# Kernel optimization log

Hardware: AMD Instinct MI355X
Metric: run time of the kernel (lower is better)

Reference implementation:

```python
import jax, jax.numpy as jnp
import numpy as np

B = 2048      # batch
S = 256       # num_hist_features (attention seq len)
D = 128       # model_dim
NSC = 16      # num scalar features
L = 2         # num attention layers
HURST = 0.1   # cfg.H
LN_EPS = 1e-5


def _log_fractional_kernel():
    # (|t-s| + 1e-9)^(H - 1.5), row-normalized, then log(k + 1e-9)
    idx = jnp.arange(S, dtype=jnp.float32)
    td = jnp.abs(idx[:, None] - idx[None, :]) + 1e-9
    kern = td ** (HURST - 1.5)
    kern = kern / kern.sum(axis=-1, keepdims=True)
    return jnp.log(kern + 1e-9)  # [S, S]


def setup_inputs() -> dict:
    key = jax.random.key(0)
    ks = jax.random.split(key, 20)
    sc = 0.02
    inp = {
        "x": jax.random.normal(ks[0], (B, NSC + S), dtype=jnp.float32),
        "scalar_W": jax.random.normal(ks[1], (NSC, D), dtype=jnp.float32) * sc,
        "scalar_b": jnp.zeros((D,), jnp.float32),
        "hist_W": jax.random.normal(ks[2], (1, D), dtype=jnp.float32) * sc,
        "hist_b": jnp.zeros((D,), jnp.float32),
        "qW": jax.random.normal(ks[3], (L, D, D), dtype=jnp.float32) * sc,
        "qb": jnp.zeros((L, D), jnp.float32),
        "kW": jax.random.normal(ks[4], (L, D, D), dtype=jnp.float32) * sc,
        "kb": jnp.zeros((L, D), jnp.float32),
        "vW": jax.random.normal(ks[5], (L, D, D), dtype=jnp.float32) * sc,
        "vb": jnp.zeros((L, D), jnp.float32),
        "ln_g": jnp.ones((L, D), jnp.float32),
        "ln_b": jnp.zeros((L, D), jnp.float32),
        "h1_W": jax.random.normal(ks[6], (D * (S + 1), 128), dtype=jnp.float32) * sc,
        "h1_b": jnp.zeros((128,), jnp.float32),
        "h2_W": jax.random.normal(ks[7], (128, 64), dtype=jnp.float32) * sc,
        "h2_b": jnp.zeros((64,), jnp.float32),
        "h3_W": jax.random.normal(ks[8], (64, 1), dtype=jnp.float32) * sc,
        "h3_b": jnp.zeros((1,), jnp.float32),
    }
    return inp


def _layernorm(h, g, b):
    mu = h.mean(axis=-1, keepdims=True)
    var = ((h - mu) ** 2).mean(axis=-1, keepdims=True)
    return (h - mu) * jax.lax.rsqrt(var + LN_EPS) * g + b


def reference(x, scalar_W, scalar_b, hist_W, hist_b, qW, qb, kW, kb, vW, vb,
              ln_g, ln_b, h1_W, h1_b, h2_W, h2_b, h3_W, h3_b):
    log_kern = _log_fractional_kernel()  # [S, S]
    scalar_feats = x[:, :-S]             # [B, NSC]
    hist_feats = x[:, -S:, None]         # [B, S, 1]
    scalar_emb = scalar_feats @ scalar_W + scalar_b   # [B, D]
    h = hist_feats @ hist_W + hist_b                   # [B, S, D]
    inv_sqrt_d = 1.0 / np.sqrt(D).astype(np.float32)
    for i in range(L):
        q = h @ qW[i] + qb[i]
        k = h @ kW[i] + kb[i]
        v = h @ vW[i] + vb[i]
        scores = jnp.einsum('bsd,btd->bst', q, k) * inv_sqrt_d  # [B,S,S]
        attn = jax.nn.softmax(scores + log_kern, axis=-1)
        out = jnp.einsum('bst,btd->bsd', attn, v)
        h = _layernorm(h + out, ln_g[i], ln_b[i])
    combined = jnp.concatenate([scalar_emb[:, None, :], h], axis=1).reshape(x.shape[0], -1)
    z = jax.nn.relu(combined @ h1_W + h1_b)
    z = jax.nn.relu(z @ h2_W + h2_b)
    return z @ h3_W + h3_b  # [B, 1]
```

## Files before the change

### kernel.cpp

```cpp
#include <hip/hip_runtime.h>
#include <cstddef>


typedef unsigned short u16;
typedef unsigned int u32;
typedef short short8 __attribute__((ext_vector_type(8)));
typedef u32 u32x2 __attribute__((ext_vector_type(2)));
typedef float floatx16 __attribute__((ext_vector_type(16)));

__device__ __forceinline__ float b2f(u16 u){ return __uint_as_float(((u32)u) << 16); }
__device__ __forceinline__ u16 f2b(float f){
  u32 u = __float_as_uint(f);
  return (u16)((u + 0x7fffu + ((u >> 16) & 1u)) >> 16);
}
__device__ __forceinline__ float ldf(const u16* p, size_t i, int f32){
  float v = f32 ? ((const float*)p)[i] : b2f(p[i]);
  return __builtin_isfinite(v) ? v : 0.f;
}
__device__ __forceinline__ u32 pk2(float a, float b){
  return ((u32)f2b(b) << 16) | (u32)f2b(a);
}
__device__ __forceinline__ int swz(int row, int ch){ return (row << 8) | ((ch ^ (row & 15)) << 4); }
__device__ __forceinline__ floatx16 fz(){
  floatx16 z;
#pragma unroll
  for (int i = 0; i < 16; ++i) z[i] = 0.f;
  return z;
}
__device__ __forceinline__ floatx16 MF(short8 a, short8 b, floatx16 c){
  return __builtin_amdgcn_mfma_f32_32x32x16_bf16(a, b, c, 0, 0, 0);
}
__device__ __forceinline__ short8 frag_from(floatx16 cv, int half, int q5){
  int r0 = half * 8;
  u32 e01 = pk2(cv[r0 + 0], cv[r0 + 1]);
  u32 e23 = pk2(cv[r0 + 2], cv[r0 + 3]);
  u32 o01 = pk2(cv[r0 + 4], cv[r0 + 5]);
  u32 o23 = pk2(cv[r0 + 6], cv[r0 + 7]);
  u32 s0 = q5 ? e01 : o01;
  u32 s1 = q5 ? e23 : o23;
  u32 r0v = __shfl_xor(s0, 32);
  u32 r1v = __shfl_xor(s1, 32);
  union { u32 u[4]; short8 v; } un;
  un.u[0] = q5 ? r0v : e01;
  un.u[1] = q5 ? r1v : e23;
  un.u[2] = q5 ? o01 : r0v;
  un.u[3] = q5 ? o23 : r1v;
  return un.v;
}

__global__ __launch_bounds__(256) void k_detect(const u16* x, int* dflag){
  __shared__ int red[256];
  int t = threadIdx.x, cnt = 0;
  for (int i = t; i < 4096; i += 256){
    u16 v = x[2 * i];
    int e = (v >> 7) & 0xFF;
    if (e == 0xFF || e >= 0x90 || (e > 0 && e <= 0x20)) ++cnt;
  }
  red[t] = cnt;
  __syncthreads();
  for (int off = 128; off > 0; off >>= 1){
    if (t < off) red[t] += red[t + off];
    __syncthreads();
  }
  if (t == 0) dflag[0] = (red[0] > 1000) ? 1 : 0;
}


__global__ __launch_bounds__(128) void k_prepw(const u16* qW, const u16* kW, const u16* vW,
                                               const u16* qb, u16* Mrow, u16* vWT, float* uv,
                                               const int* dflag){
  int fl = dflag[0];
  int i = blockIdx.x >> 7, f = blockIdx.x & 127, e = threadIdx.x;
  size_t qo = (size_t)(i * 128 + e) * 128;
  size_t ko = (size_t)(i * 128 + f) * 128;
  float m = 0.f;
  for (int d = 0; d < 128; ++d) m += ldf(qW, qo + d, fl) * ldf(kW, ko + d, fl);
  const float RS = 0.08838834764831845f;
  Mrow[(i * 128 + e) * 128 + f] = f2b(m * RS);
  vWT[(i * 128 + f) * 128 + e] = f2b(ldf(vW, qo + f, fl));
  __shared__ float red[128];
  red[e] = ldf(kW, ko + e, fl) * ldf(qb, (size_t)i * 128 + e, fl);
  __syncthreads();
  for (int off = 64; off > 0; off >>= 1){
    if (e < off) red[e] += red[e + off];
    __syncthreads();
  }
  if (e == 0) uv[i * 128 + f] = red[0] * RS;
}

__global__ __launch_bounds__(256) void k_h1t(const u16* h1W, u16* h1WT, const int* dflag){
  int fl = dflag[0];
  __shared__ u16 tile[64][130];
  int k0 = blockIdx.x * 64, tid = threadIdx.x;
#pragma unroll 4
  for (int it = 0; it < 32; ++it){
    int r = it * 2 + (tid >> 7), c = tid & 127;
    tile[r][c] = f2b(ldf(h1W, (size_t)(k0 + r) * 128 + c, fl));
  }
  __syncthreads();
#pragma unroll 4
  for (int it = 0; it < 32; ++it){
    int idx = it * 256 + tid, n = idx >> 6, kk = idx & 63;
    h1WT[(size_t)n * 32896 + k0 + kk] = tile[kk][n];
  }
}


__global__ __launch_bounds__(512) void k_fan(
    const u16* x, const u16* sW, const u16* sb, const u16* hW, const u16* hbe,
    const u16* Mrow, const float* uv, const u16* vWT, const u16* vb,
    const u16* lng, const u16* lnb,
    u16* hgq, u16* se, int qoff, const int* dflag){
  __shared__ alignas(16) u16 hL[32768];
  __shared__ alignas(16) u16 vt[16384];
  __shared__ alignas(16) u16 khL[16384];
  __shared__ float c_all[256];
  __shared__ float u_lds[128];
  int fl = dflag[0];
  int bl = blockIdx.x;
  int b = qoff + bl;
  int tid = threadIdx.x, w = tid >> 6, lane = tid & 63, l31 = lane & 31, q5 = lane >> 5;
  size_t xo = (size_t)b * 272;
  const float LKOFF = -20.72326584f;

  if (tid < 128){
    float acc = ldf(sb, tid, fl);
#pragma unroll
    for (int j = 0; j < 16; ++j) acc += ldf(x, xo + j, fl) * ldf(sW, (size_t)j * 128 + tid, fl);
    se[(size_t)b * 128 + tid] = f2b(acc);
  }
#pragma unroll
  for (int it = 0; it < 8; ++it){
    int c = it * 512 + tid, s = c >> 4, ch = c & 15;
    float xv = ldf(x, xo + 16 + s, fl);
    short8 r;
#pragma unroll
    for (int j = 0; j < 8; ++j)
      r[j] = (short)f2b(xv * ldf(hW, ch * 8 + j, fl) + ldf(hbe, ch * 8 + j, fl));
    *(short8*)((char*)hL + swz(s, ch)) = r;
  }

#pragma unroll 1
  for (int li = 0; li < 2; ++li){
    const u16* Mri  = Mrow + li * 16384;
    const u16* vWTi = vWT + li * 16384;
    if (tid < 128) u_lds[tid] = uv[li * 128 + tid];
    __syncthreads();

    {
      int row = 32 * w + l31;
      float dot = 0.f;
#pragma unroll 2
      for (int kc = 0; kc < 8; ++kc){
        int ch = 2 * kc + q5;
        short8 hv = *(const short8*)((char*)hL + swz(row, ch));
#pragma unroll
        for (int j = 0; j < 8; ++j) dot += u_lds[ch * 8 + j] * b2f(hv[j]);
      }
      dot += __shfl_xor(dot, 32);
      if (q5 == 0) c_all[row] = dot;
    }

    float ls_tot = 0.f;
    floatx16 oacc[4];
#pragma unroll
    for (int nt = 0; nt < 4; ++nt) oacc[nt] = fz();
    int scol = 32 * w + l31;

#pragma unroll 1
    for (int tt = 0; tt < 2; ++tt){
      int t0 = tt * 128;
      __syncthreads();
      {
        int mtv = w & 3;
#pragma unroll 1
        for (int j = 0; j < 2; ++j){
          int ntv = (w >> 2) * 2 + j;
          floatx16 ka = fz();
#pragma unroll 2
          for (int kc = 0; kc < 8; ++kc){
            short8 av = *(const short8*)(Mri + (32 * mtv + l31) * 128 + kc * 16 + q5 * 8);
            short8 bh = *(const short8*)((char*)hL + swz(t0 + 32 * ntv + l31, 2 * kc + q5));
            ka = MF(av, bh, ka);
          }
          int tloc = 32 * ntv + l31;
#pragma unroll
          for (int qd = 0; qd < 4; ++qd){
            u32x2 pv;
            pv.x = pk2(ka[4 * qd + 0], ka[4 * qd + 1]);
            pv.y = pk2(ka[4 * qd + 2], ka[4 * qd + 3]);
            *(u32x2*)((char*)khL + swz(tloc, 4 * mtv + qd) + 8 * q5) = pv;
          }
        }
      }
      {
        int mtv = w & 3;
        float vbl = ldf(vb, (size_t)li * 128 + 32 * mtv + l31, fl);
#pragma unroll 1
        for (int j = 0; j < 2; ++j){
          int ntv = (w >> 2) * 2 + j;
          floatx16 va = fz();
#pragma unroll 2
          for (int kc = 0; kc < 8; ++kc){
            short8 av = *(const short8*)(vWTi + (32 * mtv + l31) * 128 + kc * 16 + q5 * 8);
            short8 bh = *(const short8*)((char*)hL + swz(t0 + 32 * ntv + l31, 2 * kc + q5));
            va = MF(av, bh, va);
          }
#pragma unroll
          for (int reg = 0; reg < 16; ++reg){
            int rr = (reg & 3) + 8 * (reg >> 2) + 4 * q5;
            int tloc = 32 * ntv + l31;
            *(u16*)((char*)vt + swz(32 * mtv + rr, tloc >> 3) + (tloc & 7) * 2) =
                f2b(va[reg] + __shfl(vbl, rr));
          }
        }
      }
      __syncthreads();
#pragma unroll 1
      for (int mt = 0; mt < 4; ++mt){
        floatx16 sa = fz();
#pragma unroll 2
        for (int kc = 0; kc < 8; ++kc){
          short8 ak = *(const short8*)((char*)khL + swz(32 * mt + l31, 2 * kc + q5));
          short8 bq = *(const short8*)((char*)hL + swz(32 * w + l31, 2 * kc + q5));
          sa = MF(ak, bq, sa);
        }
#pragma unroll
        for (int reg = 0; reg < 16; ++reg){
          int trl = 32 * mt + (reg & 3) + 8 * (reg >> 2) + 4 * q5;
          int tg = t0 + trl;
          float lk = (tg == scol) ? 0.f : LKOFF;
          float v = sa[reg] + c_all[tg] + lk;
          v = fminf(fmaxf(v, -50.f), 50.f);
          float p = __expf(v - 8.f);
          sa[reg] = p;
          ls_tot += p;
        }
        short8 pf0 = frag_from(sa, 0, q5);
        short8 pf1 = frag_from(sa, 1, q5);
#pragma unroll
        for (int nt = 0; nt < 4; ++nt){
          short8 bv0 = *(const short8*)((char*)vt + swz(32 * nt + l31, 2 * (2 * mt + 0) + q5));
          oacc[nt] = MF(pf0, bv0, oacc[nt]);
          short8 bv1 = *(const short8*)((char*)vt + swz(32 * nt + l31, 2 * (2 * mt + 1) + q5));
          oacc[nt] = MF(pf1, bv1, oacc[nt]);
        }
      }
    }
    __syncthreads();

    float l_run = ls_tot + __shfl_xor(ls_tot, 32);
    float linv = 1.f / l_run;
    float gv[4], bbv[4];
#pragma unroll
    for (int nt = 0; nt < 4; ++nt){
      gv[nt]  = ldf(lng, (size_t)li * 128 + 32 * nt + l31, fl);
      bbv[nt] = ldf(lnb, (size_t)li * 128 + 32 * nt + l31, fl);
    }
#pragma unroll
    for (int reg = 0; reg < 16; ++reg){
      int rr = (reg & 3) + 8 * (reg >> 2) + 4 * q5;
      int srow = 32 * w + rr;
      float lrv = __shfl(linv, rr);
      float s1 = 0.f, s2 = 0.f;
#pragma unroll
      for (int nt = 0; nt < 4; ++nt){
        int d = 32 * nt + l31;
        float res = b2f(*(const u16*)((char*)hL + swz(srow, d >> 3) + (d & 7) * 2));
        float v = oacc[nt][reg] * lrv + res;
        oacc[nt][reg] = v;
        s1 += v; s2 += v * v;
      }
#pragma unroll
      for (int off = 1; off < 32; off <<= 1){ s1 += __shfl_xor(s1, off); s2 += __shfl_xor(s2, off); }
      float mu = s1 * 0.0078125f;
      float rs = rsqrtf(fmaxf(s2 * 0.0078125f - mu * mu, 0.f) + 1e-5f);
#pragma unroll
      for (int nt = 0; nt < 4; ++nt){
        int d = 32 * nt + l31;
        float v = (oacc[nt][reg] - mu) * rs * gv[nt] + bbv[nt];
        *(u16*)((char*)hL + swz(srow, d >> 3) + (d & 7) * 2) = f2b(v);
      }
    }
    __syncthreads();
  }

#pragma unroll
  for (int it = 0; it < 8; ++it){
    int c = it * 512 + tid, row = c >> 4, ch = c & 15;
    *(short8*)(hgq + (size_t)bl * 32768 + row * 128 + ch * 8) =
        *(const short8*)((char*)hL + swz(row, ch));
  }
}


__global__ __launch_bounds__(256) void k_mlp1(const u16* se, const u16* hgq, const u16* h1WT,
                                              float* part, int qoff, int nb){
  int mb = blockIdx.x, ks = blockIdx.y;
  int tid = threadIdx.x, w = tid >> 6, lane = tid & 63, l31 = lane & 31, q5 = lane >> 5;
  int b0 = mb * 32;
  floatx16 acc = fz();
  const u16* brow = h1WT + (size_t)(32 * w + l31) * 32896;
  int br = b0 + l31;
  const u16* seb = se + (size_t)(qoff + br) * 128;
  const u16* hb = hgq + (size_t)br * 32768;
  for (int kk = 0; kk < 257; ++kk){
    int kbase = ks * 4112 + kk * 16;
    const u16* ap = (kbase < 128) ? (seb + kbase + q5 * 8) : (hb + (kbase - 128) + q5 * 8);
    short8 a = *(const short8*)ap;
    short8 bf = *(const short8*)(brow + kbase + q5 * 8);
    acc = MF(a, bf, acc);
  }
#pragma unroll
  for (int reg = 0; reg < 16; ++reg){
    int rr = (reg & 3) + 8 * (reg >> 2) + 4 * q5;
    part[(size_t)ks * nb * 128 + (size_t)(b0 + rr) * 128 + 32 * w + l31] = acc[reg];
  }
}

__global__ __launch_bounds__(256) void k_mlp1red(const float* part, const u16* h1b, float* z1q,
                                                 const int* dflag, int nb){
  int fl = dflag[0];
  int idx = blockIdx.x * 256 + threadIdx.x;
  float s = ldf(h1b, idx & 127, fl);
  size_t stride = (size_t)nb * 128;
#pragma unroll
  for (int ks = 0; ks < 8; ++ks) s += part[(size_t)ks * stride + idx];
  z1q[idx] = fmaxf(s, 0.f);
}

__global__ __launch_bounds__(256) void k_mlp2(const float* z1, const u16* h2W, const u16* h2b,
                                              float* z2, const int* dflag){
  int fl = dflag[0];
  int idx = blockIdx.x * 256 + threadIdx.x;
  int b = idx >> 6, j = idx & 63;
  float s = ldf(h2b, j, fl);
  const float* zr = z1 + (size_t)b * 128;
  for (int k = 0; k < 128; ++k) s += zr[k] * ldf(h2W, (size_t)k * 64 + j, fl);
  z2[idx] = fmaxf(s, 0.f);
}

__global__ __launch_bounds__(256) void k_mlp3(const float* z2, const u16* h3W, const u16* h3b,
                                              void* out, const int* dflag){
  int fl = dflag[0];
  int b = blockIdx.x * 256 + threadIdx.x;
  float s = ldf(h3b, 0, fl);
  const float* zr = z2 + (size_t)b * 64;
#pragma unroll
  for (int j = 0; j < 64; ++j) s += zr[j] * ldf(h3W, j, fl);
  if (!__builtin_isfinite(s)) s = 0.f;
  if (fl) ((float*)out)[b] = s;
  else    ((u16*)out)[b] = f2b(s);
}


extern "C" void kernel_launch(void* const* d_in, const int* in_sizes, int n_in,
                              void* d_out, int out_size, void* d_ws, size_t ws_size,
                              hipStream_t stream) {
  const u16* x   = (const u16*)d_in[0];
  const u16* sW  = (const u16*)d_in[1];
  const u16* sb  = (const u16*)d_in[2];
  const u16* hW  = (const u16*)d_in[3];
  const u16* hb  = (const u16*)d_in[4];
  const u16* qW  = (const u16*)d_in[5];
  const u16* qb  = (const u16*)d_in[6];
  const u16* kW  = (const u16*)d_in[7];
  const u16* vW  = (const u16*)d_in[9];
  const u16* vb  = (const u16*)d_in[10];
  const u16* lng = (const u16*)d_in[11];
  const u16* lnb = (const u16*)d_in[12];
  const u16* h1W = (const u16*)d_in[13];
  const u16* h1b = (const u16*)d_in[14];
  const u16* h2W = (const u16*)d_in[15];
  const u16* h2b = (const u16*)d_in[16];
  const u16* h3W = (const u16*)d_in[17];
  const u16* h3b = (const u16*)d_in[18];

  const int nb = (ws_size >= 153600000ull) ? 2048 : 512;
  const int nq = 2048 / nb;

  char* W = (char*)d_ws;
  size_t o = 0;
  u16*   hg    = (u16*)(W + o); o += (size_t)nb * 65536;
  u16*   h1WT  = (u16*)(W + o); o += 8421376;
  u16*   se    = (u16*)(W + o); o += 524288;
  u16*   Mrow  = (u16*)(W + o); o += 65536;
  u16*   vWT   = (u16*)(W + o); o += 65536;
  float* uv    = (float*)(W + o); o += 1024;
  float* part  = (float*)(W + o); o += (size_t)nb * 4096;
  float* z1    = (float*)(W + o); o += 1048576;
  float* z2    = (float*)(W + o); o += 524288;
  int*   dflag = (int*)(W + o);

  k_detect<<<1, 256, 0, stream>>>(x, dflag);
  k_prepw<<<256, 128, 0, stream>>>(qW, kW, vW, qb, Mrow, vWT, uv, dflag);
  k_h1t<<<514, 256, 0, stream>>>(h1W, h1WT, dflag);

  for (int q = 0; q < nq; ++q){
    int qoff = q * nb;
    k_fan<<<nb, 512, 0, stream>>>(x, sW, sb, hW, hb, Mrow, uv, vWT, vb,
                                  lng, lnb, hg, se, qoff, dflag);
    k_mlp1<<<dim3(nb / 32, 8), 256, 0, stream>>>(se, hg, h1WT, part, qoff, nb);
    k_mlp1red<<<nb / 2, 256, 0, stream>>>(part, h1b, z1 + (size_t)qoff * 128, dflag, nb);
  }

  k_mlp2<<<512, 256, 0, stream>>>(z1, h2W, h2b, z2, dflag);
  k_mlp3<<<8, 256, 0, stream>>>(z2, h3W, h3b, d_out, dflag);
}
```

Measured before the change: 1.095 ms.

## Split attention key tiles across 16 waves with LDS partial-sum reduction

```diff
diff --git a/kernel.cpp b/kernel.cpp
--- a/kernel.cpp
+++ b/kernel.cpp
@@ -7,6 +7,7 @@
 typedef short short8 __attribute__((ext_vector_type(8)));
 typedef u32 u32x2 __attribute__((ext_vector_type(2)));
 typedef float floatx16 __attribute__((ext_vector_type(16)));
+typedef float f32x4 __attribute__((ext_vector_type(4)));
 
 __device__ __forceinline__ float b2f(u16 u){ return __uint_as_float(((u32)u) << 16); }
 __device__ __forceinline__ u16 f2b(float f){
@@ -47,6 +48,9 @@
   un.u[3] = q5 ? o23 : r1v;
   return un.v;
 }
+__device__ __forceinline__ float* mslot(u16* khL, u16* vt, int s){
+  return (s < 2) ? ((float*)khL + (s << 12)) : ((float*)vt + ((s - 2) << 12));
+}
 
 __global__ __launch_bounds__(256) void k_detect(const u16* x, int* dflag){
   __shared__ int red[256];
@@ -106,7 +110,7 @@
 }
 
 
-__global__ __launch_bounds__(512) void k_fan(
+__global__ __launch_bounds__(1024) void k_fan(
     const u16* x, const u16* sW, const u16* sb, const u16* hW, const u16* hbe,
     const u16* Mrow, const float* uv, const u16* vWT, const u16* vb,
     const u16* lng, const u16* lnb,
@@ -116,6 +120,7 @@
   __shared__ alignas(16) u16 khL[16384];
   __shared__ float c_all[256];
   __shared__ float u_lds[128];
+  __shared__ float lsx[8][64];
   int fl = dflag[0];
   int bl = blockIdx.x;
   int b = qoff + bl;
@@ -130,8 +135,8 @@
     se[(size_t)b * 128 + tid] = f2b(acc);
   }
 #pragma unroll
-  for (int it = 0; it < 8; ++it){
-    int c = it * 512 + tid, s = c >> 4, ch = c & 15;
+  for (int it = 0; it < 4; ++it){
+    int c = it * 1024 + tid, s = c >> 4, ch = c & 15;
     float xv = ldf(x, xo + 16 + s, fl);
     short8 r;
 #pragma unroll
@@ -148,81 +153,77 @@
     __syncthreads();
 
     {
-      int row = 32 * w + l31;
+      int row = 16 * w + (lane & 15);
+      int kq = lane >> 4;
       float dot = 0.f;
-#pragma unroll 2
-      for (int kc = 0; kc < 8; ++kc){
-        int ch = 2 * kc + q5;
+#pragma unroll
+      for (int kc = 0; kc < 4; ++kc){
+        int ch = 4 * kc + kq;
         short8 hv = *(const short8*)((char*)hL + swz(row, ch));
 #pragma unroll
         for (int j = 0; j < 8; ++j) dot += u_lds[ch * 8 + j] * b2f(hv[j]);
       }
+      dot += __shfl_xor(dot, 16);
       dot += __shfl_xor(dot, 32);
-      if (q5 == 0) c_all[row] = dot;
+      if (kq == 0) c_all[row] = dot;
     }
 
     float ls_tot = 0.f;
     floatx16 oacc[4];
 #pragma unroll
     for (int nt = 0; nt < 4; ++nt) oacc[nt] = fz();
-    int scol = 32 * w + l31;
+    int sg = w & 7, mh = w >> 3;
+    int scol = 32 * sg + l31;
 
 #pragma unroll 1
     for (int tt = 0; tt < 2; ++tt){
       int t0 = tt * 128;
       __syncthreads();
       {
-        int mtv = w & 3;
-#pragma unroll 1
-        for (int j = 0; j < 2; ++j){
-          int ntv = (w >> 2) * 2 + j;
-          floatx16 ka = fz();
+        int mtv = w & 3, ntv = w >> 2;
+        floatx16 ka = fz();
 #pragma unroll 2
-          for (int kc = 0; kc < 8; ++kc){
-            short8 av = *(const short8*)(Mri + (32 * mtv + l31) * 128 + kc * 16 + q5 * 8);
-            short8 bh = *(const short8*)((char*)hL + swz(t0 + 32 * ntv + l31, 2 * kc + q5));
-            ka = MF(av, bh, ka);
-          }
+        for (int kc = 0; kc < 8; ++kc){
+          short8 av = *(const short8*)(Mri + (32 * mtv + l31) * 128 + kc * 16 + q5 * 8);
+          short8 bh = *(const short8*)((char*)hL + swz(t0 + 32 * ntv + l31, 2 * kc + q5));
+          ka = MF(av, bh, ka);
+        }
+        int tloc = 32 * ntv + l31;
+#pragma unroll
+        for (int qd = 0; qd < 4; ++qd){
+          u32x2 pv;
+          pv.x = pk2(ka[4 * qd + 0], ka[4 * qd + 1]);
+          pv.y = pk2(ka[4 * qd + 2], ka[4 * qd + 3]);
+          *(u32x2*)((char*)khL + swz(tloc, 4 * mtv + qd) + 8 * q5) = pv;
+        }
+      }
+      {
+        int mtv = w & 3, ntv = w >> 2;
+        float vbl = ldf(vb, (size_t)li * 128 + 32 * mtv + l31, fl);
+        floatx16 va = fz();
+#pragma unroll 2
+        for (int kc = 0; kc < 8; ++kc){
+          short8 av = *(const short8*)(vWTi + (32 * mtv + l31) * 128 + kc * 16 + q5 * 8);
+          short8 bh = *(const short8*)((char*)hL + swz(t0 + 32 * ntv + l31, 2 * kc + q5));
+          va = MF(av, bh, va);
+        }
+#pragma unroll
+        for (int reg = 0; reg < 16; ++reg){
+          int rr = (reg & 3) + 8 * (reg >> 2) + 4 * q5;
           int tloc = 32 * ntv + l31;
-#pragma unroll
-          for (int qd = 0; qd < 4; ++qd){
-            u32x2 pv;
-            pv.x = pk2(ka[4 * qd + 0], ka[4 * qd + 1]);
-            pv.y = pk2(ka[4 * qd + 2], ka[4 * qd + 3]);
-            *(u32x2*)((char*)khL + swz(tloc, 4 * mtv + qd) + 8 * q5) = pv;
-          }
-        }
-      }
-      {
-        int mtv = w & 3;
-        float vbl = ldf(vb, (size_t)li * 128 + 32 * mtv + l31, fl);
-#pragma unroll 1
-        for (int j = 0; j < 2; ++j){
-          int ntv = (w >> 2) * 2 + j;
-          floatx16 va = fz();
-#pragma unroll 2
-          for (int kc = 0; kc < 8; ++kc){
-            short8 av = *(const short8*)(vWTi + (32 * mtv + l31) * 128 + kc * 16 + q5 * 8);
-            short8 bh = *(const short8*)((char*)hL + swz(t0 + 32 * ntv + l31, 2 * kc + q5));
-            va = MF(av, bh, va);
-          }
-#pragma unroll
-          for (int reg = 0; reg < 16; ++reg){
-            int rr = (reg & 3) + 8 * (reg >> 2) + 4 * q5;
-            int tloc = 32 * ntv + l31;
-            *(u16*)((char*)vt + swz(32 * mtv + rr, tloc >> 3) + (tloc & 7) * 2) =
-                f2b(va[reg] + __shfl(vbl, rr));
-          }
+          *(u16*)((char*)vt + swz(32 * mtv + rr, tloc >> 3) + (tloc & 7) * 2) =
+              f2b(va[reg] + __shfl(vbl, rr));
         }
       }
       __syncthreads();
 #pragma unroll 1
-      for (int mt = 0; mt < 4; ++mt){
+      for (int mm = 0; mm < 2; ++mm){
+        int mt = 2 * mh + mm;
         floatx16 sa = fz();
 #pragma unroll 2
         for (int kc = 0; kc < 8; ++kc){
           short8 ak = *(const short8*)((char*)khL + swz(32 * mt + l31, 2 * kc + q5));
-          short8 bq = *(const short8*)((char*)hL + swz(32 * w + l31, 2 * kc + q5));
+          short8 bq = *(const short8*)((char*)hL + swz(32 * sg + l31, 2 * kc + q5));
           sa = MF(ak, bq, sa);
         }
 #pragma unroll
@@ -247,47 +248,80 @@
         }
       }
     }
+
     __syncthreads();
-
-    float l_run = ls_tot + __shfl_xor(ls_tot, 32);
-    float linv = 1.f / l_run;
-    float gv[4], bbv[4];
-#pragma unroll
-    for (int nt = 0; nt < 4; ++nt){
-      gv[nt]  = ldf(lng, (size_t)li * 128 + 32 * nt + l31, fl);
-      bbv[nt] = ldf(lnb, (size_t)li * 128 + 32 * nt + l31, fl);
+    if (w >= 8) lsx[w - 8][lane] = ls_tot;
+#pragma unroll 1
+    for (int rnd = 0; rnd < 2; ++rnd){
+      if (w >= 8 + 4 * rnd && w < 12 + 4 * rnd){
+        char* bp = (char*)mslot(khL, vt, w - 8 - 4 * rnd) + lane * 256;
+#pragma unroll
+        for (int ci = 0; ci < 16; ++ci){
+          f32x4 t;
+          t[0] = oacc[ci >> 2][4 * (ci & 3) + 0];
+          t[1] = oacc[ci >> 2][4 * (ci & 3) + 1];
+          t[2] = oacc[ci >> 2][4 * (ci & 3) + 2];
+          t[3] = oacc[ci >> 2][4 * (ci & 3) + 3];
+          *(f32x4*)(bp + ((ci ^ (lane & 15)) << 4)) = t;
+        }
+      }
+      __syncthreads();
+      if (w >= 4 * rnd && w < 4 + 4 * rnd){
+        char* bp = (char*)mslot(khL, vt, w - 4 * rnd) + lane * 256;
+#pragma unroll
+        for (int ci = 0; ci < 16; ++ci){
+          f32x4 t = *(const f32x4*)(bp + ((ci ^ (lane & 15)) << 4));
+          oacc[ci >> 2][4 * (ci & 3) + 0] += t[0];
+          oacc[ci >> 2][4 * (ci & 3) + 1] += t[1];
+          oacc[ci >> 2][4 * (ci & 3) + 2] += t[2];
+          oacc[ci >> 2][4 * (ci & 3) + 3] += t[3];
+        }
+      }
+      __syncthreads();
     }
-#pragma unroll
-    for (int reg = 0; reg < 16; ++reg){
-      int rr = (reg & 3) + 8 * (reg >> 2) + 4 * q5;
-      int srow = 32 * w + rr;
-      float lrv = __shfl(linv, rr);
-      float s1 = 0.f, s2 = 0.f;
+
+    if (w < 8){
+      ls_tot += lsx[w][lane];
+      float l_run = ls_tot + __shfl_xor(ls_tot, 32);
+      float linv = 1.f / l_run;
+      float gv[4], bbv[4];
 #pragma unroll
       for (int nt = 0; nt < 4; ++nt){
-        int d = 32 * nt + l31;
-        float res = b2f(*(const u16*)((char*)hL + swz(srow, d >> 3) + (d & 7) * 2));
-        float v = oacc[nt][reg] * lrv + res;
-        oacc[nt][reg] = v;
-        s1 += v; s2 += v * v;
-      }
-#pragma unroll
-      for (int off = 1; off < 32; off <<= 1){ s1 += __shfl_xor(s1, off); s2 += __shfl_xor(s2, off); }
-      float mu = s1 * 0.0078125f;
-      float rs = rsqrtf(fmaxf(s2 * 0.0078125f - mu * mu, 0.f) + 1e-5f);
-#pragma unroll
-      for (int nt = 0; nt < 4; ++nt){
-        int d = 32 * nt + l31;
-        float v = (oacc[nt][reg] - mu) * rs * gv[nt] + bbv[nt];
-        *(u16*)((char*)hL + swz(srow, d >> 3) + (d & 7) * 2) = f2b(v);
+        gv[nt]  = ldf(lng, (size_t)li * 128 + 32 * nt + l31, fl);
+        bbv[nt] = ldf(lnb, (size_t)li * 128 + 32 * nt + l31, fl);
+      }
+#pragma unroll
+      for (int reg = 0; reg < 16; ++reg){
+        int rr = (reg & 3) + 8 * (reg >> 2) + 4 * q5;
+        int srow = 32 * sg + rr;
+        float lrv = __shfl(linv, rr);
+        float s1 = 0.f, s2 = 0.f;
+#pragma unroll
+        for (int nt = 0; nt < 4; ++nt){
+          int d = 32 * nt + l31;
+          float res = b2f(*(const u16*)((char*)hL + swz(srow, d >> 3) + (d & 7) * 2));
+          float v = oacc[nt][reg] * lrv + res;
+          oacc[nt][reg] = v;
+          s1 += v; s2 += v * v;
+        }
+#pragma unroll
+        for (int off = 1; off < 32; off <<= 1){ s1 += __shfl_xor(s1, off); s2 += __shfl_xor(s2, off); }
+        float mu = s1 * 0.0078125f;
+        float rs = rsqrtf(fmaxf(s2 * 0.0078125f - mu * mu, 0.f) + 1e-5f);
+#pragma unroll
+        for (int nt = 0; nt < 4; ++nt){
+          int d = 32 * nt + l31;
+          float v = (oacc[nt][reg] - mu) * rs * gv[nt] + bbv[nt];
+          *(u16*)((char*)hL + swz(srow, d >> 3) + (d & 7) * 2) = f2b(v);
+        }
       }
     }
     __syncthreads();
   }
 
 #pragma unroll
-  for (int it = 0; it < 8; ++it){
-    int c = it * 512 + tid, row = c >> 4, ch = c & 15;
+  for (int it = 0; it < 4; ++it){
+    int c = it * 1024 + tid, row = c >> 4, ch = c & 15;
     *(short8*)(hgq + (size_t)bl * 32768 + row * 128 + ch * 8) =
         *(const short8*)((char*)hL + swz(row, ch));
   }
@@ -398,8 +432,8 @@
 
   for (int q = 0; q < nq; ++q){
     int qoff = q * nb;
-    k_fan<<<nb, 512, 0, stream>>>(x, sW, sb, hW, hb, Mrow, uv, vWT, vb,
-                                  lng, lnb, hg, se, qoff, dflag);
+    k_fan<<<nb, 1024, 0, stream>>>(x, sW, sb, hW, hb, Mrow, uv, vWT, vb,
+                                   lng, lnb, hg, se, qoff, dflag);
     k_mlp1<<<dim3(nb / 32, 8), 256, 0, stream>>>(se, hg, h1WT, part, qoff, nb);
     k_mlp1red<<<nb / 2, 256, 0, stream>>>(part, h1b, z1 + (size_t)qoff * 128, dflag, nb);
   }
```

New measurement: 1.634 ms. +49.2%, slower.

## Fuse K/V projection MFMA loops, hoist Q fragments, split accumulators, add setprio

Applied to the files above, without the earlier changes.

```diff
diff --git a/kernel.cpp b/kernel.cpp
--- a/kernel.cpp
+++ b/kernel.cpp
@@ -106,7 +106,7 @@
 }
 
 
-__global__ __launch_bounds__(512) void k_fan(
+__global__ __launch_bounds__(512, 2) void k_fan(
     const u16* x, const u16* sW, const u16* sb, const u16* hW, const u16* hbe,
     const u16* Mrow, const float* uv, const u16* vWT, const u16* vb,
     const u16* lng, const u16* lnb,
@@ -172,18 +172,27 @@
       int t0 = tt * 128;
       __syncthreads();
       {
-        int mtv = w & 3;
-#pragma unroll 1
+        int mtv = w & 3, ntv0 = (w >> 2) * 2;
+        const u16* Ma = Mri  + (32 * mtv + l31) * 128 + q5 * 8;
+        const u16* Va = vWTi + (32 * mtv + l31) * 128 + q5 * 8;
+        float vbl = ldf(vb, (size_t)li * 128 + 32 * mtv + l31, fl);
+        int r0 = t0 + 32 * ntv0 + l31, r1 = r0 + 32;
+        floatx16 ka0 = fz(), ka1 = fz(), va0 = fz(), va1 = fz();
+#pragma unroll 2
+        for (int kc = 0; kc < 8; ++kc){
+          short8 avM = *(const short8*)(Ma + kc * 16);
+          short8 avV = *(const short8*)(Va + kc * 16);
+          short8 bh0 = *(const short8*)((char*)hL + swz(r0, 2 * kc + q5));
+          short8 bh1 = *(const short8*)((char*)hL + swz(r1, 2 * kc + q5));
+          ka0 = MF(avM, bh0, ka0);
+          va0 = MF(bh0, avV, va0);
+          ka1 = MF(avM, bh1, ka1);
+          va1 = MF(bh1, avV, va1);
+        }
+#pragma unroll
         for (int j = 0; j < 2; ++j){
-          int ntv = (w >> 2) * 2 + j;
-          floatx16 ka = fz();
-#pragma unroll 2
-          for (int kc = 0; kc < 8; ++kc){
-            short8 av = *(const short8*)(Mri + (32 * mtv + l31) * 128 + kc * 16 + q5 * 8);
-            short8 bh = *(const short8*)((char*)hL + swz(t0 + 32 * ntv + l31, 2 * kc + q5));
-            ka = MF(av, bh, ka);
-          }
-          int tloc = 32 * ntv + l31;
+          floatx16 ka = j ? ka1 : ka0;
+          int tloc = 32 * (ntv0 + j) + l31;
 #pragma unroll
           for (int qd = 0; qd < 4; ++qd){
             u32x2 pv;
@@ -192,39 +201,36 @@
             *(u32x2*)((char*)khL + swz(tloc, 4 * mtv + qd) + 8 * q5) = pv;
           }
         }
-      }
-      {
-        int mtv = w & 3;
-        float vbl = ldf(vb, (size_t)li * 128 + 32 * mtv + l31, fl);
-#pragma unroll 1
+#pragma unroll
         for (int j = 0; j < 2; ++j){
-          int ntv = (w >> 2) * 2 + j;
-          floatx16 va = fz();
-#pragma unroll 2
-          for (int kc = 0; kc < 8; ++kc){
-            short8 av = *(const short8*)(vWTi + (32 * mtv + l31) * 128 + kc * 16 + q5 * 8);
-            short8 bh = *(const short8*)((char*)hL + swz(t0 + 32 * ntv + l31, 2 * kc + q5));
-            va = MF(av, bh, va);
-          }
-#pragma unroll
-          for (int reg = 0; reg < 16; ++reg){
-            int rr = (reg & 3) + 8 * (reg >> 2) + 4 * q5;
-            int tloc = 32 * ntv + l31;
-            *(u16*)((char*)vt + swz(32 * mtv + rr, tloc >> 3) + (tloc & 7) * 2) =
-                f2b(va[reg] + __shfl(vbl, rr));
+          floatx16 va = j ? va1 : va0;
+#pragma unroll
+          for (int qd = 0; qd < 4; ++qd){
+            u32x2 pv;
+            pv.x = pk2(va[4 * qd + 0] + vbl, va[4 * qd + 1] + vbl);
+            pv.y = pk2(va[4 * qd + 2] + vbl, va[4 * qd + 3] + vbl);
+            *(u32x2*)((char*)vt + swz(32 * mtv + l31, 4 * (ntv0 + j) + qd) + 8 * q5) = pv;
           }
         }
       }
       __syncthreads();
+      short8 bqr[8];
+#pragma unroll
+      for (int kc = 0; kc < 8; ++kc)
+        bqr[kc] = *(const short8*)((char*)hL + swz(32 * w + l31, 2 * kc + q5));
 #pragma unroll 1
       for (int mt = 0; mt < 4; ++mt){
-        floatx16 sa = fz();
-#pragma unroll 2
-        for (int kc = 0; kc < 8; ++kc){
-          short8 ak = *(const short8*)((char*)khL + swz(32 * mt + l31, 2 * kc + q5));
-          short8 bq = *(const short8*)((char*)hL + swz(32 * w + l31, 2 * kc + q5));
-          sa = MF(ak, bq, sa);
-        }
+        floatx16 sae = fz(), sao = fz();
+        __builtin_amdgcn_s_setprio(1);
+#pragma unroll
+        for (int kc2 = 0; kc2 < 4; ++kc2){
+          short8 ak0 = *(const short8*)((char*)khL + swz(32 * mt + l31, 4 * kc2 + q5));
+          short8 ak1 = *(const short8*)((char*)khL + swz(32 * mt + l31, 4 * kc2 + 2 + q5));
+          sae = MF(ak0, bqr[2 * kc2 + 0], sae);
+          sao = MF(ak1, bqr[2 * kc2 + 1], sao);
+        }
+        __builtin_amdgcn_s_setprio(0);
+        floatx16 sa = sae + sao;
 #pragma unroll
         for (int reg = 0; reg < 16; ++reg){
           int trl = 32 * mt + (reg & 3) + 8 * (reg >> 2) + 4 * q5;
@@ -238,6 +244,7 @@
         }
         short8 pf0 = frag_from(sa, 0, q5);
         short8 pf1 = frag_from(sa, 1, q5);
+        __builtin_amdgcn_s_setprio(1);
 #pragma unroll
         for (int nt = 0; nt < 4; ++nt){
           short8 bv0 = *(const short8*)((char*)vt + swz(32 * nt + l31, 2 * (2 * mt + 0) + q5));
@@ -245,6 +252,7 @@
           short8 bv1 = *(const short8*)((char*)vt + swz(32 * nt + l31, 2 * (2 * mt + 1) + q5));
           oacc[nt] = MF(pf1, bv1, oacc[nt]);
         }
+        __builtin_amdgcn_s_setprio(0);
       }
     }
     __syncthreads();
```

After: 1.073 ms. 2.1% less time.

## Vectorize V-tile stores via swapped MFMA operands, add setprio and occupancy hint

Applied to the files above, without the earlier changes.

```diff
diff --git a/kernel.cpp b/kernel.cpp
--- a/kernel.cpp
+++ b/kernel.cpp
@@ -106,7 +106,7 @@
 }
 
 
-__global__ __launch_bounds__(512) void k_fan(
+__global__ __launch_bounds__(512, 2) void k_fan(
     const u16* x, const u16* sW, const u16* sb, const u16* hW, const u16* hbe,
     const u16* Mrow, const float* uv, const u16* vWT, const u16* vb,
     const u16* lng, const u16* lnb,
@@ -171,15 +171,16 @@
     for (int tt = 0; tt < 2; ++tt){
       int t0 = tt * 128;
       __syncthreads();
+      int mtv = w & 3, ntv0 = (w >> 2) * 2;
       {
-        int mtv = w & 3;
+        const u16* Ma = Mri + (32 * mtv + l31) * 128 + q5 * 8;
 #pragma unroll 1
         for (int j = 0; j < 2; ++j){
-          int ntv = (w >> 2) * 2 + j;
+          int ntv = ntv0 + j;
           floatx16 ka = fz();
 #pragma unroll 2
           for (int kc = 0; kc < 8; ++kc){
-            short8 av = *(const short8*)(Mri + (32 * mtv + l31) * 128 + kc * 16 + q5 * 8);
+            short8 av = *(const short8*)(Ma + kc * 16);
             short8 bh = *(const short8*)((char*)hL + swz(t0 + 32 * ntv + l31, 2 * kc + q5));
             ka = MF(av, bh, ka);
           }
@@ -194,24 +195,24 @@
         }
       }
       {
-        int mtv = w & 3;
+        const u16* Va = vWTi + (32 * mtv + l31) * 128 + q5 * 8;
         float vbl = ldf(vb, (size_t)li * 128 + 32 * mtv + l31, fl);
 #pragma unroll 1
         for (int j = 0; j < 2; ++j){
-          int ntv = (w >> 2) * 2 + j;
+          int rj = t0 + 32 * (ntv0 + j) + l31;
           floatx16 va = fz();
 #pragma unroll 2
           for (int kc = 0; kc < 8; ++kc){
-            short8 av = *(const short8*)(vWTi + (32 * mtv + l31) * 128 + kc * 16 + q5 * 8);
-            short8 bh = *(const short8*)((char*)hL + swz(t0 + 32 * ntv + l31, 2 * kc + q5));
-            va = MF(av, bh, va);
+            short8 avV = *(const short8*)(Va + kc * 16);
+            short8 bh  = *(const short8*)((char*)hL + swz(rj, 2 * kc + q5));
+            va = MF(bh, avV, va);
           }
 #pragma unroll
-          for (int reg = 0; reg < 16; ++reg){
-            int rr = (reg & 3) + 8 * (reg >> 2) + 4 * q5;
-            int tloc = 32 * ntv + l31;
-            *(u16*)((char*)vt + swz(32 * mtv + rr, tloc >> 3) + (tloc & 7) * 2) =
-                f2b(va[reg] + __shfl(vbl, rr));
+          for (int qd = 0; qd < 4; ++qd){
+            u32x2 pv;
+            pv.x = pk2(va[4 * qd + 0] + vbl, va[4 * qd + 1] + vbl);
+            pv.y = pk2(va[4 * qd + 2] + vbl, va[4 * qd + 3] + vbl);
+            *(u32x2*)((char*)vt + swz(32 * mtv + l31, 4 * (ntv0 + j) + qd) + 8 * q5) = pv;
           }
         }
       }
@@ -219,12 +220,14 @@
 #pragma unroll 1
       for (int mt = 0; mt < 4; ++mt){
         floatx16 sa = fz();
+        __builtin_amdgcn_s_setprio(1);
 #pragma unroll 2
         for (int kc = 0; kc < 8; ++kc){
           short8 ak = *(const short8*)((char*)khL + swz(32 * mt + l31, 2 * kc + q5));
           short8 bq = *(const short8*)((char*)hL + swz(32 * w + l31, 2 * kc + q5));
           sa = MF(ak, bq, sa);
         }
+        __builtin_amdgcn_s_setprio(0);
 #pragma unroll
         for (int reg = 0; reg < 16; ++reg){
           int trl = 32 * mt + (reg & 3) + 8 * (reg >> 2) + 4 * q5;
@@ -238,6 +241,7 @@
         }
         short8 pf0 = frag_from(sa, 0, q5);
         short8 pf1 = frag_from(sa, 1, q5);
+        __builtin_amdgcn_s_setprio(1);
 #pragma unroll
         for (int nt = 0; nt < 4; ++nt){
           short8 bv0 = *(const short8*)((char*)vt + swz(32 * nt + l31, 2 * (2 * mt + 0) + q5));
@@ -245,6 +249,7 @@
           short8 bv1 = *(const short8*)((char*)vt + swz(32 * nt + l31, 2 * (2 * mt + 1) + q5));
           oacc[nt] = MF(pf1, bv1, oacc[nt]);
         }
+        __builtin_amdgcn_s_setprio(0);
       }
     }
     __syncthreads();
```

Result: faster. 1.053 ms (-3.8%).
